# Kernel tuning notes

Hardware: AMD Instinct MI355X
Metric: run time of the kernel (lower is better)

The kernel has to match this reference:

```python
import jax, jax.numpy as jnp
import numpy as np

NMOL, NATOM, NPAIR = 32, 512, 32768
NBASIS, HIDDEN, NSPEC = 64, 256, 8
RC = 5.0
TOTNATOM = NMOL * NATOM


def setup_inputs() -> dict:
    key = jax.random.key(0)
    ks = jax.random.split(key, 8)
    cart = jax.random.normal(ks[0], (NMOL, NATOM, 3), jnp.float32) * 3.0
    shifts = jax.random.normal(ks[1], (NMOL, NPAIR, 3), jnp.float32) * 0.1
    species = jax.random.randint(ks[2], (NMOL, NATOM), 0, NSPEC)
    atom_index = jax.random.randint(ks[3], (2, NMOL, NPAIR), 0, NATOM)
    numatoms = jnp.full((NMOL,), NATOM, jnp.int32)
    centers = jnp.linspace(0.0, RC, NBASIS).astype(jnp.float32)
    widths = jnp.full((NBASIS,), 0.5, jnp.float32)
    c_emb = jax.random.normal(ks[4], (NSPEC, NBASIS), jnp.float32)
    W1 = jax.random.normal(ks[5], (NBASIS, HIDDEN), jnp.float32) / np.sqrt(NBASIS).astype(np.float32)
    b1 = jnp.zeros((HIDDEN,), jnp.float32)
    W2 = jax.random.normal(ks[6], (HIDDEN, 1), jnp.float32) / np.sqrt(HIDDEN).astype(np.float32)
    b2 = jnp.zeros((1,), jnp.float32)
    return dict(cart=cart, shifts=shifts, centers=centers, widths=widths, c_emb=c_emb,
                W1=W1, b1=b1, W2=W2, b2=b2,
                numatoms=numatoms, species=species, atom_index=atom_index)


def reference(cart, shifts, centers, widths, c_emb, W1, b1, W2, b2, numatoms, species, atom_index):
    species_flat = species.reshape(-1)                      # [totnatom]
    cart_flat = cart.reshape(-1, 3)                         # [totnatom, 3]
    # per-molecule atom offset, expanded over pairs (matches self_mol_index)
    mol_off = (jnp.arange(NMOL, dtype=atom_index.dtype) * NATOM)  # [nmol]
    off = jnp.broadcast_to(mol_off[:, None], (NMOL, NPAIR)).reshape(-1)  # [npairs_tot]
    idx12 = atom_index.reshape(2, -1) + off[None, :]        # [2, npairs_tot]
    shifts_flat = shifts.reshape(-1, 3)
    # padding mask (torch code drops rows with shift == -1e10; we mask instead)
    valid = jnp.all(shifts_flat > -1e10, axis=1)
    mask_f = valid.astype(cart.dtype)                       # [npairs_tot]
    # gather pair coords, periodic-shifted displacement
    c0 = cart_flat[idx12[0]]                                # [npairs_tot, 3]
    c1 = cart_flat[idx12[1]]
    dist_vec = (c0 - c1 + shifts_flat) * mask_f[:, None]    # [npairs_tot, 3]
    d = jnp.sqrt(jnp.sum(dist_vec * dist_vec, axis=1) + 1e-12)  # safe norm
    # embedded density: gaussian RBF * cosine cutoff * neighbor-species coeff
    rbf = jnp.exp(-widths[None, :] * (d[:, None] - centers[None, :]) ** 2)  # [P, nbasis]
    fc = 0.5 * (jnp.cos(jnp.pi * d / RC) + 1.0) * (d < RC).astype(cart.dtype)
    pair_feat = rbf * (fc * mask_f)[:, None] * c_emb[species_flat[idx12[1]]]
    density = jax.ops.segment_sum(pair_feat, idx12[0], num_segments=TOTNATOM)  # [totnatom, nbasis]
    # per-atom scalar output (nnmod)
    h = jax.nn.silu(density @ W1 + b1)
    output = (h @ W2 + b2).reshape(-1)                      # [totnatom]
    # scatter-add displacement vectors to center atom
    tot_vec = jax.ops.segment_sum(dist_vec, idx12[0], num_segments=TOTNATOM)  # [totnatom, 3]
    # weighted contraction ('i,ij->ij') + per-molecule sum -> dipole
    dipole = jnp.sum((output[:, None] * tot_vec).reshape(NMOL, NATOM, 3), axis=1)  # [nmol, 3]
    return dipole
```

## Files before the change

kernel.cpp:

```cpp
#include <hip/hip_runtime.h>

#define NMOL   32
#define NATOM  512
#define NPAIR  32768
#define NB     64
#define HIDDEN 256
#define TOTNATOM (NMOL * NATOM)
#define NSUB   8
#define BLKCAP4 4352
#define BLKCAP2 2816
#define ABLK   4
#define NSLOT  48

typedef __attribute__((ext_vector_type(8))) short bf16x8;
typedef __attribute__((ext_vector_type(4))) float f32x4;

__device__ __forceinline__ unsigned short f2bf(float x) {
    unsigned u = __float_as_uint(x);
    u += 0x7FFFu + ((u >> 16) & 1u);
    return (unsigned short)(u >> 16);
}

__global__ __launch_bounds__(1024) void scatter_kernel(
    const float* __restrict__ cart, const float* __restrict__ shifts,
    const int* __restrict__ species, const int* __restrict__ atom_index,
    unsigned* __restrict__ cnt, unsigned* __restrict__ soff_g,
    float2* __restrict__ rec, float* __restrict__ tv_part,
    float* __restrict__ dipole, int ndip)
{
    __shared__ float    s_cart[NATOM * 3];
    __shared__ int      s_sp[NATOM];
    __shared__ unsigned lcnt[NATOM];
    __shared__ unsigned pref[NATOM];
    __shared__ unsigned ccnt[NATOM];
    __shared__ unsigned pref2[NATOM];
    __shared__ float    lx[BLKCAP4];
    __shared__ float    ly[BLKCAP4];
    __shared__ float    lz[BLKCAP4];

    const int tid  = threadIdx.x;
    const int lane = tid & 63;
    const int wave = tid >> 6;
    const int b    = blockIdx.x;
    const int mol  = b & 31;
    const int sub  = b >> 5;

    if (b == 0 && tid < ndip) dipole[tid] = 0.f;

    const float* cm = cart + (size_t)mol * NATOM * 3;
    const int*   sp = species + (size_t)mol * NATOM;
    for (int i = tid; i < NATOM * 3; i += 1024) s_cart[i] = cm[i];
    if (tid < NATOM) { lcnt[tid] = 0u; s_sp[tid] = sp[tid]; }
    __syncthreads();

    const int* ai0 = atom_index + (size_t)mol * NPAIR;
    const int* ai1 = ai0 + (size_t)NMOL * NPAIR;
    const float* sh = shifts + (size_t)mol * NPAIR * 3;
    const int base = sub * 4096;

    int   gi0[4], gi1[4];
    float gsx[4], gsy[4], gsz[4];
#pragma unroll
    for (int k = 0; k < 4; ++k) {
        const int p = base + k * 1024 + tid;
        gi0[k] = ai0[p];
        gi1[k] = ai1[p];
        gsx[k] = sh[p * 3 + 0];
        gsy[k] = sh[p * 3 + 1];
        gsz[k] = sh[p * 3 + 2];
    }

    float    rx[4], ry[4], rz[4];
    unsigned rs[4], rp[4];
    int      ri[4];
#pragma unroll
    for (int k = 0; k < 4; ++k) {
        const int a3 = gi0[k] * 3, b3 = gi1[k] * 3;
        const bool m = (gsx[k] > -1e10f && gsy[k] > -1e10f && gsz[k] > -1e10f);
        ri[k] = -1;
        if (m) {
            rx[k] = s_cart[a3 + 0] - s_cart[b3 + 0] + gsx[k];
            ry[k] = s_cart[a3 + 1] - s_cart[b3 + 1] + gsy[k];
            rz[k] = s_cart[a3 + 2] - s_cart[b3 + 2] + gsz[k];
            rs[k] = (unsigned)s_sp[gi1[k]];
            ri[k] = gi0[k];
            rp[k] = atomicAdd(&lcnt[gi0[k]], 1u);
        }
    }
    __syncthreads();

    if (wave == 0) {
        unsigned c[8], s = 0;
#pragma unroll
        for (int j = 0; j < 8; ++j) { c[j] = lcnt[lane * 8 + j]; s += c[j]; }
        unsigned incl = s;
#pragma unroll
        for (int off = 1; off < 64; off <<= 1) {
            const unsigned v = __shfl_up(incl, off);
            if (lane >= off) incl += v;
        }
        unsigned run = incl - s;
#pragma unroll
        for (int j = 0; j < 8; ++j) { pref[lane * 8 + j] = run; run += c[j]; }
    }
    __syncthreads();

#pragma unroll
    for (int k = 0; k < 4; ++k) {
        if (ri[k] >= 0) {
            const unsigned idx = pref[ri[k]] + rp[k];
            if (idx < (unsigned)BLKCAP4) {
                lx[idx] = rx[k];
                ly[idx] = ry[k];
                lz[idx] = __uint_as_float((__float_as_uint(rz[k]) & ~7u) | rs[k]);
            }
        }
    }
    __syncthreads();

    if (tid < NATOM) {
        const int a  = tid;
        const int j0 = (int)pref[a];
        const int j1 = min(j0 + (int)lcnt[a], BLKCAP4);
        float tx = 0.f, ty = 0.f, tz = 0.f;
        unsigned c2 = 0;
        for (int j = j0; j < j1; ++j) {
            const float x = lx[j], y = ly[j], z = lz[j];
            tx += x; ty += y; tz += z;
            const float d = sqrtf(x * x + y * y + z * z + 1e-12f);
            if (d < 5.0f) ++c2;
        }
        ccnt[a] = c2;
        float* tg = tv_part + ((size_t)b * NATOM + a) * 3;
        tg[0] = tx; tg[1] = ty; tg[2] = tz;
    }
    __syncthreads();

    if (wave == 0) {
        unsigned c[8], s = 0;
#pragma unroll
        for (int j = 0; j < 8; ++j) { c[j] = ccnt[lane * 8 + j]; s += c[j]; }
        unsigned incl = s;
#pragma unroll
        for (int off = 1; off < 64; off <<= 1) {
            const unsigned v = __shfl_up(incl, off);
            if (lane >= off) incl += v;
        }
        unsigned run = incl - s;
#pragma unroll
        for (int j = 0; j < 8; ++j) { pref2[lane * 8 + j] = run; run += c[j]; }
    }
    __syncthreads();

    if (tid < NATOM) {
        const int a  = tid;
        const int j0 = (int)pref[a];
        const int j1 = min(j0 + (int)lcnt[a], BLKCAP4);
        unsigned w = pref2[a];
        float2* dstr = rec + (size_t)b * BLKCAP2;
        for (int j = j0; j < j1; ++j) {
            const float x = lx[j], y = ly[j], z = lz[j];
            const float d = sqrtf(x * x + y * y + z * z + 1e-12f);
            if (d < 5.0f) {
                const float fc = 0.5f * (__cosf(0.62831853071795864769f * d) + 1.f);
                const unsigned fb = (__float_as_uint(fc) & ~7u)
                                  | (__float_as_uint(z) & 7u);
                if (w < (unsigned)BLKCAP2)
                    dstr[w] = make_float2(d, __uint_as_float(fb));
                ++w;
            }
        }
        cnt[((size_t)mol * NATOM + a) * NSUB + sub] = ccnt[a];
        soff_g[(size_t)b * NATOM + a] = pref2[a];
    }
}

__global__ __launch_bounds__(256) void gather_kernel(
    const unsigned* __restrict__ cnt, const unsigned* __restrict__ soff_g,
    const float2* __restrict__ rec,
    const float* __restrict__ centers, const float* __restrict__ widths,
    const float* __restrict__ c_emb, const float* __restrict__ tv_part,
    unsigned short* __restrict__ dens_bf, float* __restrict__ tvv)
{
    __shared__ float    cemb[8 * NB];
    __shared__ float2   list2[ABLK][NSLOT];
    __shared__ unsigned scnt[ABLK][NSUB];
    __shared__ unsigned sofg[ABLK][NSUB];
    __shared__ unsigned soff[ABLK][NSUB];
    __shared__ unsigned mtot[ABLK];

    const int tid   = threadIdx.x;
    const int B     = blockIdx.x;
    const int mol   = B & 31;
    const int inner = B >> 5;
    const int a0    = mol * NATOM + inner * ABLK;
    const int ra0   = inner * ABLK;

    for (int i = tid; i < 8 * NB; i += 256) cemb[i] = c_emb[i];
    if (tid < ABLK * NSUB) {
        const int al = tid >> 3, s = tid & 7;
        scnt[al][s] = cnt[(size_t)(a0 + al) * NSUB + s];
        sofg[al][s] = soff_g[(size_t)(s * NMOL + mol) * NATOM + (ra0 + al)];
    }
    __syncthreads();

    if (tid < ABLK) {
        int o = 0;
#pragma unroll
        for (int s = 0; s < NSUB; ++s) {
            soff[tid][s] = (unsigned)o;
            o += min((int)scnt[tid][s], NSLOT - o);
        }
        const int mp = (o + 7) & ~7;
        mtot[tid] = (unsigned)(mp <= NSLOT ? mp : NSLOT & ~7);
        for (int k = o; k < mp && k < NSLOT; ++k)
            list2[tid][k] = make_float2(0.f, 0.f);
    }
    __syncthreads();

    {
        const int seg = tid >> 3;
        const int prt = tid & 7;
        const int al = seg >> 3, s = seg & 7;
        const int off = (int)soff[al][s];
        const int n = min((int)scnt[al][s], NSLOT - off);
        const float2* src = rec + (size_t)(s * NMOL + mol) * BLKCAP2 + sofg[al][s];
        float2* dst = &list2[al][off];
        for (int k = prt; k < n; k += 8) dst[k] = src[k];
    }
    if (tid < ABLK * 3) {
        const int al = tid / 3, c = tid - al * 3;
        float s = 0.f;
#pragma unroll
        for (int sb = 0; sb < NSUB; ++sb)
            s += tv_part[((size_t)(sb * NMOL + mol) * NATOM + (ra0 + al)) * 3 + c];
        tvv[(size_t)(a0 + al) * 3 + c] = s;
    }
    __syncthreads();

    const int lane = tid & 63;
    const int al   = tid >> 6;
    const int a    = a0 + al;

    const float L2E = 1.4426950408889634f;
    const float wl  = widths[lane];
    const float cl  = centers[lane];
    const float qe  = -wl * L2E;
    const float qb  = 2.f * wl * cl * L2E;
    const float qa  = -wl * cl * cl * L2E;

#define REC1(A, dv, fv) { const unsigned f_ = __float_as_uint(fv);           \
        const float v_ = fmaf(dv, fmaf(dv, qe, qb), qa);                     \
        A = fmaf(exp2f(v_) * __uint_as_float(f_ & ~7u),                      \
                 cemb[((f_ & 7u) << 6) | lane], A); }
    const int mp = (int)mtot[al];
    const float4* l4 = reinterpret_cast<const float4*>(list2[al]);
    float acc0 = 0.f, acc1 = 0.f;
    for (int j = 0; j < mp; j += 8) {
        const float4 q0 = l4[(j >> 1) + 0];
        const float4 q1 = l4[(j >> 1) + 1];
        const float4 q2 = l4[(j >> 1) + 2];
        const float4 q3 = l4[(j >> 1) + 3];
        REC1(acc0, q0.x, q0.y) REC1(acc1, q0.z, q0.w)
        REC1(acc0, q1.x, q1.y) REC1(acc1, q1.z, q1.w)
        REC1(acc0, q2.x, q2.y) REC1(acc1, q2.z, q2.w)
        REC1(acc0, q3.x, q3.y) REC1(acc1, q3.z, q3.w)
    }
#undef REC1
    dens_bf[(size_t)a * NB + lane] = f2bf(acc0 + acc1);
}

__global__ __launch_bounds__(256) void nn_kernel(
    const unsigned short* __restrict__ dens_bf, const float* __restrict__ tvv,
    const float* __restrict__ W1, const float* __restrict__ b1,
    const float* __restrict__ W2, const float* __restrict__ b2,
    float* __restrict__ dipole)
{
    __shared__ __align__(16) unsigned short w1t[HIDDEN * 72];
    __shared__ float b1_l[HIDDEN], w2_l[HIDDEN];
    __shared__ float sred[4][4][3];

    const int tid   = threadIdx.x;
    const int B     = blockIdx.x;
    const int mol   = B & 31;
    const int chunk = B >> 5;

    for (int i = tid; i < NB * HIDDEN; i += 256) {
        const int k = i >> 8, j = i & 255;
        w1t[j * 72 + k] = f2bf(W1[i]);
    }
    if (tid < HIDDEN) { b1_l[tid] = b1[tid]; w2_l[tid] = W2[tid]; }
    __syncthreads();

    const int lane = tid & 63;
    const int wave = tid >> 6;
    const int fr   = lane & 15;
    const int fg   = lane >> 4;
    const int a0w  = mol * NATOM + chunk * 64 + wave * 16;

    bf16x8 afr[2];
#pragma unroll
    for (int kk = 0; kk < 2; ++kk)
        afr[kk] = *reinterpret_cast<const bf16x8*>(
            dens_bf + (size_t)(a0w + fr) * NB + kk * 32 + fg * 8);

    float sdip[4] = {0.f, 0.f, 0.f, 0.f};
#pragma unroll
    for (int nt = 0; nt < 16; ++nt) {
        const bf16x8 bf0 = *reinterpret_cast<const bf16x8*>(
            &w1t[(nt * 16 + fr) * 72 + 0 + fg * 8]);
        const bf16x8 bf1 = *reinterpret_cast<const bf16x8*>(
            &w1t[(nt * 16 + fr) * 72 + 32 + fg * 8]);
        f32x4 acc = {0.f, 0.f, 0.f, 0.f};
        acc = __builtin_amdgcn_mfma_f32_16x16x32_bf16(afr[0], bf0, acc, 0, 0, 0);
        acc = __builtin_amdgcn_mfma_f32_16x16x32_bf16(afr[1], bf1, acc, 0, 0, 0);
        const int j = nt * 16 + fr;
        const float b1v = b1_l[j], w2v = w2_l[j];
#pragma unroll
        for (int i = 0; i < 4; ++i) {
            const float h = acc[i] + b1v;
            sdip[i] += (h / (1.f + __expf(-h))) * w2v;
        }
    }
#pragma unroll
    for (int off = 1; off < 16; off <<= 1) {
#pragma unroll
        for (int i = 0; i < 4; ++i) sdip[i] += __shfl_xor(sdip[i], off);
    }
    if (fr == 0) {
        const float b2v = b2[0];
        float px = 0.f, py = 0.f, pz = 0.f;
#pragma unroll
        for (int i = 0; i < 4; ++i) {
            const int a = a0w + fg * 4 + i;
            const float out = sdip[i] + b2v;
            px += out * tvv[a * 3 + 0];
            py += out * tvv[a * 3 + 1];
            pz += out * tvv[a * 3 + 2];
        }
        sred[wave][fg][0] = px; sred[wave][fg][1] = py; sred[wave][fg][2] = pz;
    }
    __syncthreads();
    if (tid < 3) {
        float s = 0.f;
#pragma unroll
        for (int w = 0; w < 4; ++w)
#pragma unroll
            for (int g = 0; g < 4; ++g) s += sred[w][g][tid];
        unsafeAtomicAdd(&dipole[mol * 3 + tid], s);
    }
}

extern "C" void kernel_launch(void* const* d_in, const int* in_sizes, int n_in,
                              void* d_out, int out_size, void* d_ws, size_t ws_size,
                              hipStream_t stream)
{
    const float* cart       = (const float*)d_in[0];
    const float* shifts     = (const float*)d_in[1];
    const float* centers    = (const float*)d_in[2];
    const float* widths     = (const float*)d_in[3];
    const float* c_emb      = (const float*)d_in[4];
    const float* W1         = (const float*)d_in[5];
    const float* b1         = (const float*)d_in[6];
    const float* W2         = (const float*)d_in[7];
    const float* b2         = (const float*)d_in[8];
    const int*   species    = (const int*)d_in[10];
    const int*   atom_index = (const int*)d_in[11];

    unsigned*       cnt     = (unsigned*)d_ws;
    unsigned*       soff_g  = cnt + (size_t)TOTNATOM * NSUB;
    float*          tvv     = (float*)(soff_g + (size_t)NMOL * NSUB * NATOM);
    float*          tv_part = tvv + (size_t)TOTNATOM * 3;
    unsigned short* dens_bf = (unsigned short*)(tv_part + (size_t)NMOL * NSUB * NATOM * 3);
    float2*         rec     = (float2*)(dens_bf + (size_t)TOTNATOM * NB);
    float*          dipole  = (float*)d_out;

    hipLaunchKernelGGL(scatter_kernel, dim3(NMOL * NSUB), dim3(1024), 0, stream,
                       cart, shifts, species, atom_index, cnt, soff_g, rec,
                       tv_part, dipole, out_size);
    hipLaunchKernelGGL(gather_kernel, dim3(TOTNATOM / ABLK), dim3(256), 0, stream,
                       cnt, soff_g, rec, centers, widths, c_emb, tv_part,
                       dens_bf, tvv);
    hipLaunchKernelGGL(nn_kernel, dim3(TOTNATOM / 64), dim3(256), 0, stream,
                       dens_bf, tvv, W1, b1, W2, b2, dipole);
}
```

Before: 40.35 us.

## Fuse density gather and MLP into one kernel with LDS-resident densities

Merges the per-atom density gather and the MLP/dipole kernel into one kernel where each block handles 64 atoms of one molecule in two halves. Densities and summed displacement vectors stay in LDS instead of going through global memory, and one kernel launch is removed. The trade is a much smaller grid (256 blocks versus thousands) with each wave looping over eight atoms and serial per-thread list copies, which lowers parallelism in the gather phase.

```diff
diff --git a/kernel.cpp b/kernel.cpp
--- a/kernel.cpp
+++ b/kernel.cpp
@@ -9,7 +9,6 @@
 #define NSUB   8
 #define BLKCAP4 4352
 #define BLKCAP2 2816
-#define ABLK   4
 #define NSLOT  48
 
 typedef __attribute__((ext_vector_type(8))) short bf16x8;
@@ -175,73 +174,43 @@
     }
 }
 
-__global__ __launch_bounds__(256) void gather_kernel(
+__global__ __launch_bounds__(256) void gnn_kernel(
     const unsigned* __restrict__ cnt, const unsigned* __restrict__ soff_g,
     const float2* __restrict__ rec,
     const float* __restrict__ centers, const float* __restrict__ widths,
     const float* __restrict__ c_emb, const float* __restrict__ tv_part,
-    unsigned short* __restrict__ dens_bf, float* __restrict__ tvv)
+    const float* __restrict__ W1, const float* __restrict__ b1,
+    const float* __restrict__ W2, const float* __restrict__ b2,
+    float* __restrict__ dipole)
 {
+    __shared__ __align__(16) unsigned short w1t[HIDDEN * 72];
+    __shared__ float    b1_l[HIDDEN], w2_l[HIDDEN];
     __shared__ float    cemb[8 * NB];
-    __shared__ float2   list2[ABLK][NSLOT];
-    __shared__ unsigned scnt[ABLK][NSUB];
-    __shared__ unsigned sofg[ABLK][NSUB];
-    __shared__ unsigned soff[ABLK][NSUB];
-    __shared__ unsigned mtot[ABLK];
+    __shared__ __align__(16) unsigned short dens_l[64][72];
+    __shared__ float    tv_l[64 * 3];
+    __shared__ float2   list2[32][NSLOT];
+    __shared__ unsigned scnt[32][NSUB];
+    __shared__ unsigned sofg[32][NSUB];
+    __shared__ unsigned soff[32][NSUB];
+    __shared__ unsigned mtot[32];
+    __shared__ float    sred[4][4][3];
 
     const int tid   = threadIdx.x;
     const int B     = blockIdx.x;
     const int mol   = B & 31;
-    const int inner = B >> 5;
-    const int a0    = mol * NATOM + inner * ABLK;
-    const int ra0   = inner * ABLK;
-
+    const int chunk = B >> 5;
+    const int a0    = mol * NATOM + chunk * 64;
+    const int ra0   = chunk * 64;
+
+    for (int i = tid; i < NB * HIDDEN; i += 256) {
+        const int k = i >> 8, j = i & 255;
+        w1t[j * 72 + k] = f2bf(W1[i]);
+    }
+    if (tid < HIDDEN) { b1_l[tid] = b1[tid]; w2_l[tid] = W2[tid]; }
     for (int i = tid; i < 8 * NB; i += 256) cemb[i] = c_emb[i];
-    if (tid < ABLK * NSUB) {
-        const int al = tid >> 3, s = tid & 7;
-        scnt[al][s] = cnt[(size_t)(a0 + al) * NSUB + s];
-        sofg[al][s] = soff_g[(size_t)(s * NMOL + mol) * NATOM + (ra0 + al)];
-    }
-    __syncthreads();
-
-    if (tid < ABLK) {
-        int o = 0;
-#pragma unroll
-        for (int s = 0; s < NSUB; ++s) {
-            soff[tid][s] = (unsigned)o;
-            o += min((int)scnt[tid][s], NSLOT - o);
-        }
-        const int mp = (o + 7) & ~7;
-        mtot[tid] = (unsigned)(mp <= NSLOT ? mp : NSLOT & ~7);
-        for (int k = o; k < mp && k < NSLOT; ++k)
-            list2[tid][k] = make_float2(0.f, 0.f);
-    }
-    __syncthreads();
-
-    {
-        const int seg = tid >> 3;
-        const int prt = tid & 7;
-        const int al = seg >> 3, s = seg & 7;
-        const int off = (int)soff[al][s];
-        const int n = min((int)scnt[al][s], NSLOT - off);
-        const float2* src = rec + (size_t)(s * NMOL + mol) * BLKCAP2 + sofg[al][s];
-        float2* dst = &list2[al][off];
-        for (int k = prt; k < n; k += 8) dst[k] = src[k];
-    }
-    if (tid < ABLK * 3) {
-        const int al = tid / 3, c = tid - al * 3;
-        float s = 0.f;
-#pragma unroll
-        for (int sb = 0; sb < NSUB; ++sb)
-            s += tv_part[((size_t)(sb * NMOL + mol) * NATOM + (ra0 + al)) * 3 + c];
-        tvv[(size_t)(a0 + al) * 3 + c] = s;
-    }
-    __syncthreads();
 
     const int lane = tid & 63;
-    const int al   = tid >> 6;
-    const int a    = a0 + al;
-
+    const int wave = tid >> 6;
     const float L2E = 1.4426950408889634f;
     const float wl  = widths[lane];
     const float cl  = centers[lane];
@@ -249,105 +218,130 @@
     const float qb  = 2.f * wl * cl * L2E;
     const float qa  = -wl * cl * cl * L2E;
 
+    for (int half = 0; half < 2; ++half) {
+        const int ab = half * 32;
+        __syncthreads();
+
+        {
+            const int al = tid >> 3, s = tid & 7;
+            scnt[al][s] = cnt[(size_t)(a0 + ab + al) * NSUB + s];
+            sofg[al][s] = soff_g[(size_t)(s * NMOL + mol) * NATOM + (ra0 + ab + al)];
+        }
+        __syncthreads();
+
+        if (tid < 32) {
+            int o = 0;
+#pragma unroll
+            for (int s = 0; s < NSUB; ++s) {
+                soff[tid][s] = (unsigned)o;
+                o += min((int)scnt[tid][s], NSLOT - o);
+            }
+            const int mp = (o + 7) & ~7;
+            mtot[tid] = (unsigned)(mp <= NSLOT ? mp : NSLOT & ~7);
+            for (int k = o; k < mp && k < NSLOT; ++k)
+                list2[tid][k] = make_float2(0.f, 0.f);
+        }
+        if (tid >= 128 && tid < 128 + 96) {
+            const int t = tid - 128;
+            const int al = t / 3, c = t - al * 3;
+            float s = 0.f;
+#pragma unroll
+            for (int sb = 0; sb < NSUB; ++sb)
+                s += tv_part[((size_t)(sb * NMOL + mol) * NATOM + (ra0 + ab + al)) * 3 + c];
+            tv_l[(ab + al) * 3 + c] = s;
+        }
+        __syncthreads();
+
+        {
+            const int al = tid >> 3, s = tid & 7;
+            const int off = (int)soff[al][s];
+            const int n = min((int)scnt[al][s], NSLOT - off);
+            const float2* src = rec + (size_t)(s * NMOL + mol) * BLKCAP2 + sofg[al][s];
+            float2* dst = &list2[al][off];
+            for (int k = 0; k < n; ++k) dst[k] = src[k];
+        }
+        __syncthreads();
+
 #define REC1(A, dv, fv) { const unsigned f_ = __float_as_uint(fv);           \
         const float v_ = fmaf(dv, fmaf(dv, qe, qb), qa);                     \
         A = fmaf(exp2f(v_) * __uint_as_float(f_ & ~7u),                      \
                  cemb[((f_ & 7u) << 6) | lane], A); }
-    const int mp = (int)mtot[al];
-    const float4* l4 = reinterpret_cast<const float4*>(list2[al]);
-    float acc0 = 0.f, acc1 = 0.f;
-    for (int j = 0; j < mp; j += 8) {
-        const float4 q0 = l4[(j >> 1) + 0];
-        const float4 q1 = l4[(j >> 1) + 1];
-        const float4 q2 = l4[(j >> 1) + 2];
-        const float4 q3 = l4[(j >> 1) + 3];
-        REC1(acc0, q0.x, q0.y) REC1(acc1, q0.z, q0.w)
-        REC1(acc0, q1.x, q1.y) REC1(acc1, q1.z, q1.w)
-        REC1(acc0, q2.x, q2.y) REC1(acc1, q2.z, q2.w)
-        REC1(acc0, q3.x, q3.y) REC1(acc1, q3.z, q3.w)
-    }
+        for (int al = wave; al < 32; al += 4) {
+            const int mp = (int)mtot[al];
+            const float4* l4 = reinterpret_cast<const float4*>(list2[al]);
+            float acc0 = 0.f, acc1 = 0.f;
+            for (int j = 0; j < mp; j += 8) {
+                const float4 q0 = l4[(j >> 1) + 0];
+                const float4 q1 = l4[(j >> 1) + 1];
+                const float4 q2 = l4[(j >> 1) + 2];
+                const float4 q3 = l4[(j >> 1) + 3];
+                REC1(acc0, q0.x, q0.y) REC1(acc1, q0.z, q0.w)
+                REC1(acc0, q1.x, q1.y) REC1(acc1, q1.z, q1.w)
+                REC1(acc0, q2.x, q2.y) REC1(acc1, q2.z, q2.w)
+                REC1(acc0, q3.x, q3.y) REC1(acc1, q3.z, q3.w)
+            }
+            dens_l[ab + al][lane] = f2bf(acc0 + acc1);
+        }
 #undef REC1
-    dens_bf[(size_t)a * NB + lane] = f2bf(acc0 + acc1);
-}
-
-__global__ __launch_bounds__(256) void nn_kernel(
-    const unsigned short* __restrict__ dens_bf, const float* __restrict__ tvv,
-    const float* __restrict__ W1, const float* __restrict__ b1,
-    const float* __restrict__ W2, const float* __restrict__ b2,
-    float* __restrict__ dipole)
-{
-    __shared__ __align__(16) unsigned short w1t[HIDDEN * 72];
-    __shared__ float b1_l[HIDDEN], w2_l[HIDDEN];
-    __shared__ float sred[4][4][3];
-
-    const int tid   = threadIdx.x;
-    const int B     = blockIdx.x;
-    const int mol   = B & 31;
-    const int chunk = B >> 5;
-
-    for (int i = tid; i < NB * HIDDEN; i += 256) {
-        const int k = i >> 8, j = i & 255;
-        w1t[j * 72 + k] = f2bf(W1[i]);
-    }
-    if (tid < HIDDEN) { b1_l[tid] = b1[tid]; w2_l[tid] = W2[tid]; }
-    __syncthreads();
-
-    const int lane = tid & 63;
-    const int wave = tid >> 6;
-    const int fr   = lane & 15;
-    const int fg   = lane >> 4;
-    const int a0w  = mol * NATOM + chunk * 64 + wave * 16;
-
-    bf16x8 afr[2];
-#pragma unroll
-    for (int kk = 0; kk < 2; ++kk)
-        afr[kk] = *reinterpret_cast<const bf16x8*>(
-            dens_bf + (size_t)(a0w + fr) * NB + kk * 32 + fg * 8);
-
-    float sdip[4] = {0.f, 0.f, 0.f, 0.f};
-#pragma unroll
-    for (int nt = 0; nt < 16; ++nt) {
-        const bf16x8 bf0 = *reinterpret_cast<const bf16x8*>(
-            &w1t[(nt * 16 + fr) * 72 + 0 + fg * 8]);
-        const bf16x8 bf1 = *reinterpret_cast<const bf16x8*>(
-            &w1t[(nt * 16 + fr) * 72 + 32 + fg * 8]);
-        f32x4 acc = {0.f, 0.f, 0.f, 0.f};
-        acc = __builtin_amdgcn_mfma_f32_16x16x32_bf16(afr[0], bf0, acc, 0, 0, 0);
-        acc = __builtin_amdgcn_mfma_f32_16x16x32_bf16(afr[1], bf1, acc, 0, 0, 0);
-        const int j = nt * 16 + fr;
-        const float b1v = b1_l[j], w2v = w2_l[j];
-#pragma unroll
-        for (int i = 0; i < 4; ++i) {
-            const float h = acc[i] + b1v;
-            sdip[i] += (h / (1.f + __expf(-h))) * w2v;
-        }
-    }
-#pragma unroll
-    for (int off = 1; off < 16; off <<= 1) {
-#pragma unroll
-        for (int i = 0; i < 4; ++i) sdip[i] += __shfl_xor(sdip[i], off);
-    }
-    if (fr == 0) {
-        const float b2v = b2[0];
-        float px = 0.f, py = 0.f, pz = 0.f;
-#pragma unroll
-        for (int i = 0; i < 4; ++i) {
-            const int a = a0w + fg * 4 + i;
-            const float out = sdip[i] + b2v;
-            px += out * tvv[a * 3 + 0];
-            py += out * tvv[a * 3 + 1];
-            pz += out * tvv[a * 3 + 2];
-        }
-        sred[wave][fg][0] = px; sred[wave][fg][1] = py; sred[wave][fg][2] = pz;
-    }
-    __syncthreads();
-    if (tid < 3) {
-        float s = 0.f;
-#pragma unroll
-        for (int w = 0; w < 4; ++w)
-#pragma unroll
-            for (int g = 0; g < 4; ++g) s += sred[w][g][tid];
-        unsafeAtomicAdd(&dipole[mol * 3 + tid], s);
+    }
+    __syncthreads();
+
+    {
+        const int fr = lane & 15;
+        const int fg = lane >> 4;
+        const int lbase = wave * 16;
+
+        bf16x8 afr[2];
+#pragma unroll
+        for (int kk = 0; kk < 2; ++kk)
+            afr[kk] = *reinterpret_cast<const bf16x8*>(
+                &dens_l[lbase + fr][kk * 32 + fg * 8]);
+
+        float sdip[4] = {0.f, 0.f, 0.f, 0.f};
+#pragma unroll
+        for (int nt = 0; nt < 16; ++nt) {
+            const bf16x8 bf0 = *reinterpret_cast<const bf16x8*>(
+                &w1t[(nt * 16 + fr) * 72 + 0 + fg * 8]);
+            const bf16x8 bf1 = *reinterpret_cast<const bf16x8*>(
+                &w1t[(nt * 16 + fr) * 72 + 32 + fg * 8]);
+            f32x4 acc = {0.f, 0.f, 0.f, 0.f};
+            acc = __builtin_amdgcn_mfma_f32_16x16x32_bf16(afr[0], bf0, acc, 0, 0, 0);
+            acc = __builtin_amdgcn_mfma_f32_16x16x32_bf16(afr[1], bf1, acc, 0, 0, 0);
+            const int j = nt * 16 + fr;
+            const float b1v = b1_l[j], w2v = w2_l[j];
+#pragma unroll
+            for (int i = 0; i < 4; ++i) {
+                const float h = acc[i] + b1v;
+                sdip[i] += (h / (1.f + __expf(-h))) * w2v;
+            }
+        }
+#pragma unroll
+        for (int off = 1; off < 16; off <<= 1) {
+#pragma unroll
+            for (int i = 0; i < 4; ++i) sdip[i] += __shfl_xor(sdip[i], off);
+        }
+        if (fr == 0) {
+            const float b2v = b2[0];
+            float px = 0.f, py = 0.f, pz = 0.f;
+#pragma unroll
+            for (int i = 0; i < 4; ++i) {
+                const int la = lbase + fg * 4 + i;
+                const float out = sdip[i] + b2v;
+                px += out * tv_l[la * 3 + 0];
+                py += out * tv_l[la * 3 + 1];
+                pz += out * tv_l[la * 3 + 2];
+            }
+            sred[wave][fg][0] = px; sred[wave][fg][1] = py; sred[wave][fg][2] = pz;
+        }
+        __syncthreads();
+        if (tid < 3) {
+            float s = 0.f;
+#pragma unroll
+            for (int w = 0; w < 4; ++w)
+#pragma unroll
+                for (int g = 0; g < 4; ++g) s += sred[w][g][tid];
+            unsafeAtomicAdd(&dipole[mol * 3 + tid], s);
+        }
     }
 }
 
@@ -367,20 +361,16 @@
     const int*   species    = (const int*)d_in[10];
     const int*   atom_index = (const int*)d_in[11];
 
-    unsigned*       cnt     = (unsigned*)d_ws;
-    unsigned*       soff_g  = cnt + (size_t)TOTNATOM * NSUB;
-    float*          tvv     = (float*)(soff_g + (size_t)NMOL * NSUB * NATOM);
-    float*          tv_part = tvv + (size_t)TOTNATOM * 3;
-    unsigned short* dens_bf = (unsigned short*)(tv_part + (size_t)NMOL * NSUB * NATOM * 3);
-    float2*         rec     = (float2*)(dens_bf + (size_t)TOTNATOM * NB);
-    float*          dipole  = (float*)d_out;
+    unsigned* cnt     = (unsigned*)d_ws;
+    unsigned* soff_g  = cnt + (size_t)TOTNATOM * NSUB;
+    float*    tv_part = (float*)(soff_g + (size_t)NMOL * NSUB * NATOM);
+    float2*   rec     = (float2*)(tv_part + (size_t)NMOL * NSUB * NATOM * 3);
+    float*    dipole  = (float*)d_out;
 
     hipLaunchKernelGGL(scatter_kernel, dim3(NMOL * NSUB), dim3(1024), 0, stream,
                        cart, shifts, species, atom_index, cnt, soff_g, rec,
                        tv_part, dipole, out_size);
-    hipLaunchKernelGGL(gather_kernel, dim3(TOTNATOM / ABLK), dim3(256), 0, stream,
+    hipLaunchKernelGGL(gnn_kernel, dim3(NMOL * NSUB), dim3(256), 0, stream,
                        cnt, soff_g, rec, centers, widths, c_emb, tv_part,
-                       dens_bf, tvv);
-    hipLaunchKernelGGL(nn_kernel, dim3(TOTNATOM / 64), dim3(256), 0, stream,
-                       dens_bf, tvv, W1, b1, W2, b2, dipole);
+                       W1, b1, W2, b2, dipole);
 }
```

Measured after the change: 50.72 us. 1.26x slower.
